# Optimization experiments

Measured on AMD Instinct MI355X. Metric: run time of the kernel, lower is better.

The kernel has to match this reference:

```python
import jax, jax.numpy as jnp
import numpy as np

EPS_LN = 1e-5

def _ln(x, g, b):
    m = x.mean(-1, keepdims=True)
    v = jnp.var(x, axis=-1, keepdims=True)
    return (x - m) * jax.lax.rsqrt(v + EPS_LN) * g + b


def _forward(x, edge_attr, lin0_w, lin0_b, enn_w1, enn_b1, enn_g1, enn_b1n,
             enn_w2, enn_b2, enn_g2, enn_b2n, conv_bias,
             gru_w_ih, gru_w_hh, gru_b_ih, gru_b_hh,
             lstm_w_ih, lstm_w_hh, lstm_b_ih, lstm_b_hh,
             lin1_w, lin1_b, lin1_g, lin1_bn, lin2_w, lin2_b,
             edge_index, target_index, target_class):
    N = x.shape[0]
    D = lin0_w.shape[0]
    src, dst = edge_index[0], edge_index[1]

    out = jax.nn.relu(x @ lin0_w.T + lin0_b)            # [N, D]
    h = out                                             # GRU hidden state

    # edge NN -> per-edge weight matrix [E, D, D] (edge_attr constant across iters)
    e1 = jax.nn.relu(_ln(edge_attr @ enn_w1.T + enn_b1, enn_g1, enn_b1n))
    ew = _ln(e1 @ enn_w2.T + enn_b2, enn_g2, enn_b2n).reshape(-1, D, D)

    counts = jnp.clip(jax.ops.segment_sum(jnp.ones_like(dst, jnp.float32), dst, num_segments=N), 1.0)[:, None]

    for _ in range(3):
        msg = jnp.einsum('ed,edo->eo', out[src], ew)     # per-edge matmul
        agg = jax.ops.segment_sum(msg, dst, num_segments=N) / counts  # scatter-mean
        m = jax.nn.relu(agg + conv_bias)
        # GRU cell (seq len 1)
        gx = m @ gru_w_ih.T + gru_b_ih
        gh = h @ gru_w_hh.T + gru_b_hh
        xr, xz, xn = jnp.split(gx, 3, axis=-1)
        hr, hz, hn = jnp.split(gh, 3, axis=-1)
        r = jax.nn.sigmoid(xr + hr)
        z = jax.nn.sigmoid(xz + hz)
        n = jnp.tanh(xn + r * hn)
        h = (1.0 - z) * n + z * h
        out = h

    # Set2Set with batch_index = arange(N) (each node is its own set), 3 steps
    idx = jnp.arange(N)
    hl = jnp.zeros((N, D), x.dtype)
    cl = jnp.zeros((N, D), x.dtype)
    q_star = jnp.zeros((N, 2 * D), x.dtype)
    for _ in range(3):
        g = q_star @ lstm_w_ih.T + lstm_b_ih + hl @ lstm_w_hh.T + lstm_b_hh
        gi, gf, gg, go = jnp.split(g, 4, axis=-1)
        cl = jax.nn.sigmoid(gf) * cl + jax.nn.sigmoid(gi) * jnp.tanh(gg)
        hl = jax.nn.sigmoid(go) * jnp.tanh(cl)
        q = hl
        e = (out * q[idx]).sum(-1, keepdims=True)
        emax = jax.ops.segment_max(e, idx, num_segments=N)
        a = jnp.exp(e - emax[idx])
        a = a / (jax.ops.segment_sum(a, idx, num_segments=N)[idx] + 1e-16)
        r_pool = jax.ops.segment_sum(a * out, idx, num_segments=N)
        q_star = jnp.concatenate([q, r_pool], axis=-1)

    a0, a1 = target_index[0], target_index[1]
    cat = jnp.concatenate([out[a0], out[a1], q_star[a0], q_star[a1]], axis=-1)  # [P, 6D]
    p = jax.nn.relu(_ln(cat @ lin1_w.T + lin1_b, lin1_g, lin1_bn))
    p = p @ lin2_w.T + lin2_b                           # [P, 8]
    return jnp.take_along_axis(p, target_class[:, None], axis=1)[:, 0]


def setup_inputs() -> dict:
    N, E, P, F, D = 10000, 20000, 15000, 16, 64
    ks = iter(jax.random.split(jax.random.key(0), 40))
    def nrm(shape, s=0.1):
        return jax.random.normal(next(ks), shape, jnp.float32) * s
    return {
        'x': jax.random.normal(next(ks), (N, F), jnp.float32),
        'edge_attr': jax.random.normal(next(ks), (E, 4), jnp.float32),
        'lin0_w': nrm((D, F)), 'lin0_b': jnp.zeros((D,), jnp.float32),
        'enn_w1': nrm((128, 4)), 'enn_b1': jnp.zeros((128,), jnp.float32),
        'enn_g1': jnp.ones((128,), jnp.float32), 'enn_b1n': jnp.zeros((128,), jnp.float32),
        'enn_w2': nrm((D * D, 128), 0.05), 'enn_b2': jnp.zeros((D * D,), jnp.float32),
        'enn_g2': jnp.ones((D * D,), jnp.float32), 'enn_b2n': jnp.zeros((D * D,), jnp.float32),
        'conv_bias': jnp.zeros((D,), jnp.float32),
        'gru_w_ih': nrm((3 * D, D)), 'gru_w_hh': nrm((3 * D, D)),
        'gru_b_ih': jnp.zeros((3 * D,), jnp.float32), 'gru_b_hh': jnp.zeros((3 * D,), jnp.float32),
        'lstm_w_ih': nrm((4 * D, 2 * D)), 'lstm_w_hh': nrm((4 * D, D)),
        'lstm_b_ih': jnp.zeros((4 * D,), jnp.float32), 'lstm_b_hh': jnp.zeros((4 * D,), jnp.float32),
        'lin1_w': nrm((D, 6 * D)), 'lin1_b': jnp.zeros((D,), jnp.float32),
        'lin1_g': jnp.ones((D,), jnp.float32), 'lin1_bn': jnp.zeros((D,), jnp.float32),
        'lin2_w': nrm((8, D)), 'lin2_b': jnp.zeros((8,), jnp.float32),
        'edge_index': jax.random.randint(next(ks), (2, E), 0, N),
        'target_index': jax.random.randint(next(ks), (2, P), 0, N),
        'target_class': jax.random.randint(next(ks), (P,), 0, 8),
    }


def reference(x, edge_attr, lin0_w, lin0_b, enn_w1, enn_b1, enn_g1, enn_b1n,
              enn_w2, enn_b2, enn_g2, enn_b2n, conv_bias,
              gru_w_ih, gru_w_hh, gru_b_ih, gru_b_hh,
              lstm_w_ih, lstm_w_hh, lstm_b_ih, lstm_b_hh,
              lin1_w, lin1_b, lin1_g, lin1_bn, lin2_w, lin2_b,
              edge_index, target_index, target_class):
    return _forward(x, edge_attr, lin0_w, lin0_b, enn_w1, enn_b1, enn_g1, enn_b1n,
                    enn_w2, enn_b2, enn_g2, enn_b2n, conv_bias,
                    gru_w_ih, gru_w_hh, gru_b_ih, gru_b_hh,
                    lstm_w_ih, lstm_w_hh, lstm_b_ih, lstm_b_hh,
                    lin1_w, lin1_b, lin1_g, lin1_bn, lin2_w, lin2_b,
                    edge_index, target_index, target_class)
```

## Files before the change

kernel.cpp:

```cpp
#include <hip/hip_runtime.h>
#include <hip/hip_bf16.h>

#define EPS_LN 1e-5f

typedef __attribute__((ext_vector_type(8))) short bf16x8;
typedef __attribute__((ext_vector_type(4))) float f32x4;

__device__ __forceinline__ float dot4(float4 a, float4 b) {
    return a.x * b.x + a.y * b.y + a.z * b.z + a.w * b.w;
}
__device__ __forceinline__ float sigmoidf_(float x) { return 1.0f / (1.0f + expf(-x)); }

__device__ __forceinline__ float bfu2f(unsigned short u) {
    unsigned v = ((unsigned)u) << 16;
    float f;
    __builtin_memcpy(&f, &v, 4);
    return f;
}
__device__ __forceinline__ unsigned short f2bfu(float f) {
    __hip_bfloat16 h = __float2bfloat16(f);
    unsigned short u;
    __builtin_memcpy(&u, &h, 2);
    return u;
}
__device__ __forceinline__ unsigned pack2bf(float a, float b) {
    return (unsigned)f2bfu(a) | ((unsigned)f2bfu(b) << 16);
}

__global__ void init_kernel(const float* __restrict__ x, const float* __restrict__ w,
                            const float* __restrict__ b, float* __restrict__ h,
                            const int* __restrict__ ei, float* __restrict__ counts,
                            int N, int E) {
    int id = blockIdx.x * blockDim.x + threadIdx.x;
    if (id < N * 64) {
        int n = id >> 6, o = id & 63;
        const float* xr = x + n * 16;
        const float* wr = w + o * 16;
        float acc = b[o];
#pragma unroll
        for (int k = 0; k < 16; k++) acc += xr[k] * wr[k];
        h[id] = fmaxf(acc, 0.0f);
    }
    if (id < E) atomicAdd(&counts[ei[E + id]], 1.0f);
}

__global__ __launch_bounds__(128) void edge_nn1_kernel(
    const float* __restrict__ ea, const float* __restrict__ w1, const float* __restrict__ b1,
    const float* __restrict__ g1, const float* __restrict__ b1n,
    unsigned short* __restrict__ e1h, unsigned short* __restrict__ e1l, int E) {
    int e = blockIdx.x, j = threadIdx.x;
    float a0 = ea[e * 4 + 0], a1 = ea[e * 4 + 1], a2 = ea[e * 4 + 2], a3 = ea[e * 4 + 3];
    const float* wr = w1 + j * 4;
    float z = b1[j] + a0 * wr[0] + a1 * wr[1] + a2 * wr[2] + a3 * wr[3];
    float s = z, s2 = z * z;
#pragma unroll
    for (int m = 32; m >= 1; m >>= 1) { s += __shfl_xor(s, m); s2 += __shfl_xor(s2, m); }
    __shared__ float ls[2], ls2[2];
    int wv = j >> 6;
    if ((j & 63) == 0) { ls[wv] = s; ls2[wv] = s2; }
    __syncthreads();
    float S = ls[0] + ls[1], S2 = ls2[0] + ls2[1];
    float mu = S * (1.0f / 128.0f);
    float var = fmaxf(S2 * (1.0f / 128.0f) - mu * mu, 0.0f);
    float inv = rsqrtf(var + EPS_LN);
    float v = fmaxf((z - mu) * inv * g1[j] + b1n[j], 0.0f);
    unsigned short hi = f2bfu(v);
    unsigned short lo = f2bfu(v - bfu2f(hi));
    e1h[e * 128 + j] = hi;
    e1l[e * 128 + j] = lo;
}

__global__ __launch_bounds__(128) void mpart_kernel(const float* __restrict__ w2,
                                                    const float* __restrict__ b2,
                                                    const float* __restrict__ g2,
                                                    unsigned short* __restrict__ w2g,
                                                    float* __restrict__ b2g,
                                                    float* __restrict__ pMT, float* __restrict__ pv,
                                                    float* __restrict__ pcw, float* __restrict__ psb,
                                                    float* __restrict__ pc) {
    __shared__ float wL[16][128];
    __shared__ float b2L[16];
    int t = threadIdx.x, b = blockIdx.x;
#pragma unroll
    for (int i = 0; i < 16; i++) {
        int idx = t + i * 128;
        wL[idx >> 7][idx & 127] = w2[(size_t)(b * 16 + (idx >> 7)) * 128 + (idx & 127)];
    }
    if (t < 16) b2L[t] = b2[b * 16 + t];
    __syncthreads();
#pragma unroll
    for (int o = 0; o < 16; o++) {
        int row = b * 16 + o;
        w2g[(size_t)row * 128 + t] = f2bfu(wL[o][t] * g2[row]);
    }
    if (t < 16) b2g[b * 16 + t] = b2L[t] * g2[b * 16 + t];
    int j = t;
    float wj[16];
#pragma unroll
    for (int o = 0; o < 16; o++) wj[o] = wL[o][j];
    float pvj = 0.f, pcwj = 0.f;
#pragma unroll
    for (int o = 0; o < 16; o++) { pvj += wj[o] * b2L[o]; pcwj += wj[o]; }
    for (int i4 = 0; i4 < 32; i4++) {
        float4 a = {0.f, 0.f, 0.f, 0.f};
#pragma unroll
        for (int o = 0; o < 16; o++) {
            float4 w4 = *(const float4*)&wL[o][i4 * 4];
            a.x += wj[o] * w4.x; a.y += wj[o] * w4.y;
            a.z += wj[o] * w4.z; a.w += wj[o] * w4.w;
        }
        *(float4*)&pMT[((size_t)b * 128 + j) * 128 + i4 * 4] = a;
    }
    pv[b * 128 + j] = pvj;
    pcw[b * 128 + j] = pcwj;
    if (t == 0) {
        float sb = 0.f, cc = 0.f;
#pragma unroll
        for (int o = 0; o < 16; o++) { sb += b2L[o]; cc += b2L[o] * b2L[o]; }
        psb[b] = sb;
        pc[b] = cc;
    }
}

__global__ __launch_bounds__(256) void mreduce_kernel(const float* __restrict__ pMT,
                                                      const float* __restrict__ pv,
                                                      const float* __restrict__ pcw,
                                                      const float* __restrict__ psb,
                                                      const float* __restrict__ pc,
                                                      unsigned short* __restrict__ mb,
                                                      float* __restrict__ varr,
                                                      float* __restrict__ cw,
                                                      float* __restrict__ sbc) {
    int fid = blockIdx.x * 256 + threadIdx.x;
    float s = 0.f;
    int j = fid >> 7, i = fid & 127;
    for (int b = 0; b < 256; b++) s += pMT[((size_t)b * 128 + j) * 128 + i];
    mb[fid] = f2bfu(s);
    if (fid < 128) {
        float sv = 0.f, sc = 0.f;
        for (int b = 0; b < 256; b++) { sv += pv[b * 128 + fid]; sc += pcw[b * 128 + fid]; }
        varr[fid] = sv;
        cw[fid] = sc;
    }
    if (fid == 0) {
        float sb = 0.f, cc = 0.f;
        for (int b = 0; b < 256; b++) { sb += psb[b]; cc += pc[b]; }
        sbc[0] = sb;
        sbc[1] = cc;
    }
}

__global__ __launch_bounds__(256) void stats_kernel(
    const unsigned short* __restrict__ e1h, const unsigned short* __restrict__ e1l,
    const unsigned short* __restrict__ mb, const float* __restrict__ cw,
    const float* __restrict__ varr, const float* __restrict__ sbc,
    float* __restrict__ stats, int E) {
    __shared__ __align__(16) unsigned char smem[65536];
    const int t = threadIdx.x;
    const int eb = blockIdx.x * 64;
#pragma unroll
    for (int r = 0; r < 4; r++) {
        int idx = t + r * 256;
        int row = idx >> 4, kseg = idx & 15;
        int er = eb + row;
        if (er >= E) er = E - 1;
        uint4 vh = *(const uint4*)&e1h[(size_t)er * 128 + kseg * 8];
        uint4 vl = *(const uint4*)&e1l[(size_t)er * 128 + kseg * 8];
        int off = row * 256 + ((kseg * 16) ^ ((row & 7) << 4));
        *(uint4*)(smem + off) = vh;
        *(uint4*)(smem + 16384 + off) = vl;
    }
#pragma unroll
    for (int r = 0; r < 8; r++) {
        int idx = t + r * 256;
        int row = idx >> 4, kseg = idx & 15;
        uint4 v = *(const uint4*)&mb[(size_t)row * 128 + kseg * 8];
        *(uint4*)(smem + 32768 + row * 256 + ((kseg * 16) ^ ((row & 7) << 4))) = v;
    }
    __syncthreads();
    const int w = t >> 6, lane = t & 63;
    const int wrow = w * 16;
    const int r16 = lane & 15, kg = lane >> 4;
    f32x4 tacc[8];
#pragma unroll
    for (int nj = 0; nj < 8; nj++) tacc[nj] = (f32x4){0.f, 0.f, 0.f, 0.f};
#pragma unroll
    for (int ks = 0; ks < 4; ks++) {
        int arow = wrow + r16;
        int koff = ks * 64 + kg * 16;
        bf16x8 ah = *(const bf16x8*)(smem + arow * 256 + (koff ^ ((arow & 7) << 4)));
        bf16x8 al = *(const bf16x8*)(smem + 16384 + arow * 256 + (koff ^ ((arow & 7) << 4)));
#pragma unroll
        for (int nj = 0; nj < 8; nj++) {
            int brow = nj * 16 + r16;
            bf16x8 bf = *(const bf16x8*)(smem + 32768 + brow * 256 + (koff ^ ((brow & 7) << 4)));
            tacc[nj] = __builtin_amdgcn_mfma_f32_16x16x32_bf16(ah, bf, tacc[nj], 0, 0, 0);
            tacc[nj] = __builtin_amdgcn_mfma_f32_16x16x32_bf16(al, bf, tacc[nj], 0, 0, 0);
        }
    }
    __syncthreads();
#pragma unroll
    for (int nj = 0; nj < 8; nj++)
#pragma unroll
        for (int r = 0; r < 4; r++) {
            int row = wrow + kg * 4 + r, col = nj * 16 + r16;
            *(float*)(smem + 32768 + row * 512 + col * 4) = tacc[nj][r];
        }
    __syncthreads();
    int el = t >> 2, q = t & 3;
    float s2p = 0.f, sp = 0.f, svp = 0.f;
    for (int kk = 0; kk < 32; kk++) {
        int k = q * 32 + kk;
        int boff = el * 256 + ((2 * k) ^ ((el & 7) << 4));
        float e1v = bfu2f(*(const unsigned short*)(smem + boff)) +
                    bfu2f(*(const unsigned short*)(smem + 16384 + boff));
        float tv = *(const float*)(smem + 32768 + el * 512 + k * 4);
        s2p += tv * e1v;
        sp += e1v * cw[k];
        svp += e1v * varr[k];
    }
    s2p += __shfl_xor(s2p, 1); s2p += __shfl_xor(s2p, 2);
    sp += __shfl_xor(sp, 1);   sp += __shfl_xor(sp, 2);
    svp += __shfl_xor(svp, 1); svp += __shfl_xor(svp, 2);
    if (q == 0) {
        int e = eb + el;
        if (e < E) {
            float S = sp + sbc[0];
            float S2 = s2p + 2.f * svp + sbc[1];
            float mu = S * (1.0f / 4096.0f);
            float var = fmaxf(S2 * (1.0f / 4096.0f) - mu * mu, 0.0f);
            float inv = rsqrtf(var + EPS_LN);
            stats[e * 2 + 0] = inv;
            stats[e * 2 + 1] = mu * inv;
        }
    }
}

__global__ __launch_bounds__(256) void zgemm_final(
    const unsigned short* __restrict__ e1h,
    const unsigned short* __restrict__ w2g, const float* __restrict__ b2g,
    const float* __restrict__ g2, const float* __restrict__ b2n,
    const float* __restrict__ stats, unsigned short* __restrict__ zT, int E) {
    __shared__ __align__(16) unsigned char smem[49152];
    __shared__ float cBg[128], cGg[128], cBn[128];
    __shared__ float sInv[64], sMiv[64];
    const int t = threadIdx.x;
    const int eb = blockIdx.y * 64;
    const int cb = blockIdx.x * 128;
    const int o0 = blockIdx.x * 2;
#pragma unroll
    for (int r = 0; r < 4; r++) {
        int idx = t + r * 256;
        int row = idx >> 4, kseg = idx & 15;
        int er = eb + row;
        if (er >= E) er = E - 1;
        uint4 vh = *(const uint4*)&e1h[(size_t)er * 128 + kseg * 8];
        *(uint4*)(smem + row * 256 + ((kseg * 16) ^ ((row & 7) << 4))) = vh;
    }
#pragma unroll
    for (int r = 0; r < 8; r++) {
        int idx = t + r * 256;
        int j = idx >> 4, kseg = idx & 15;
        int srcrow = ((j & 63) << 6) + o0 + (j >> 6);
        uint4 v = *(const uint4*)&w2g[(size_t)srcrow * 128 + kseg * 8];
        *(uint4*)(smem + 16384 + j * 256 + ((kseg * 16) ^ ((j & 7) << 4))) = v;
    }
    if (t < 128) {
        int sj = ((t & 63) << 6) + o0 + (t >> 6);
        cBg[t] = b2g[sj];
        cGg[t] = g2[sj];
        cBn[t] = b2n[sj];
    } else if (t < 192) {
        int tt = t - 128;
        int eg = eb + tt;
        if (eg >= E) eg = E - 1;
        sInv[tt] = stats[eg * 2 + 0];
        sMiv[tt] = stats[eg * 2 + 1];
    }
    __syncthreads();
    const int w = t >> 6, lane = t & 63;
    const int wrow = (w >> 1) * 32, wcol = (w & 1) * 64;
    const int r16 = lane & 15, kg = lane >> 4;

    f32x4 acc[2][4];
#pragma unroll
    for (int mi = 0; mi < 2; mi++)
#pragma unroll
        for (int nj = 0; nj < 4; nj++) acc[mi][nj] = (f32x4){0.f, 0.f, 0.f, 0.f};
#pragma unroll
    for (int ks = 0; ks < 4; ks++) {
        int koff = ks * 64 + kg * 16;
        bf16x8 af[2];
#pragma unroll
        for (int mi = 0; mi < 2; mi++) {
            int row = wrow + mi * 16 + r16;
            af[mi] = *(const bf16x8*)(smem + row * 256 + (koff ^ ((row & 7) << 4)));
        }
        bf16x8 bf[4];
#pragma unroll
        for (int nj = 0; nj < 4; nj++) {
            int row = wcol + nj * 16 + r16;
            bf[nj] = *(const bf16x8*)(smem + 16384 + row * 256 + (koff ^ ((row & 7) << 4)));
        }
#pragma unroll
        for (int mi = 0; mi < 2; mi++)
#pragma unroll
            for (int nj = 0; nj < 4; nj++)
                acc[mi][nj] = __builtin_amdgcn_mfma_f32_16x16x32_bf16(
                    bf[nj], af[mi], acc[mi][nj], 0, 0, 0);
    }
#pragma unroll
    for (int mi = 0; mi < 2; mi++) {
        int e_local = wrow + mi * 16 + r16;
        int e = eb + e_local;
        float inv = sInv[e_local], miv = sMiv[e_local];
        bool ok = (e < E);
#pragma unroll
        for (int nj = 0; nj < 4; nj++) {
            int j0 = wcol + nj * 16 + kg * 4;
            float4 bg4 = *(const float4*)&cBg[j0];
            float4 gg4 = *(const float4*)&cGg[j0];
            float4 bn4 = *(const float4*)&cBn[j0];
            ushort4 sv;
            sv.x = f2bfu(inv * (acc[mi][nj][0] + bg4.x) - miv * gg4.x + bn4.x);
            sv.y = f2bfu(inv * (acc[mi][nj][1] + bg4.y) - miv * gg4.y + bn4.y);
            sv.z = f2bfu(inv * (acc[mi][nj][2] + bg4.z) - miv * gg4.z + bn4.z);
            sv.w = f2bfu(inv * (acc[mi][nj][3] + bg4.w) - miv * gg4.w + bn4.w);
            if (ok) *(ushort4*)&zT[(size_t)e * 4096 + cb + j0] = sv;
        }
    }
}

__global__ __launch_bounds__(256) void msg_kernel(const unsigned short* __restrict__ zT,
                                                  const float* __restrict__ h,
                                                  const int* __restrict__ ei,
                                                  float* __restrict__ agg, int E) {
    int t = threadIdx.x;
    int el = t >> 6, o = t & 63;
    int e = blockIdx.x * 4 + el;
    __shared__ float sL[4][64];
    int src = ei[e];
    int dstn = ei[E + e];
    sL[el][o] = h[src * 64 + o];
    __syncthreads();
    float acc = 0.f;
    const uint4* zp = (const uint4*)(zT + (size_t)e * 4096 + o * 64);
#pragma unroll
    for (int q = 0; q < 8; q++) {
        uint4 v = zp[q];
        const float* hp = &sL[el][q * 8];
        acc += __uint_as_float(v.x << 16) * hp[0] + __uint_as_float(v.x & 0xffff0000u) * hp[1];
        acc += __uint_as_float(v.y << 16) * hp[2] + __uint_as_float(v.y & 0xffff0000u) * hp[3];
        acc += __uint_as_float(v.z << 16) * hp[4] + __uint_as_float(v.z & 0xffff0000u) * hp[5];
        acc += __uint_as_float(v.w << 16) * hp[6] + __uint_as_float(v.w & 0xffff0000u) * hp[7];
    }
    atomicAdd(&agg[(size_t)dstn * 64 + o], acc);
}

__global__ __launch_bounds__(192) void gru_kernel(
    const float* __restrict__ agg, const float* __restrict__ counts, const float* __restrict__ cbias,
    const float* __restrict__ wih, const float* __restrict__ whh,
    const float* __restrict__ bih, const float* __restrict__ bhh, float* __restrict__ h, int N) {
    int t = threadIdx.x;
    int nb = blockIdx.x * 8;
    __shared__ __align__(16) float mL[8][64], hL[8][64], gxL[8][192], ghL[8][192];
    for (int idx = t; idx < 512; idx += 192) {
        int n = idx >> 6, k = idx & 63;
        int node = nb + n;
        float cnt = fmaxf(counts[node], 1.0f);
        mL[n][k] = fmaxf(agg[node * 64 + k] / cnt + cbias[k], 0.0f);
        hL[n][k] = h[node * 64 + k];
    }
    __syncthreads();
    {
        int j = t;
        float ax[8], ah[8];
#pragma unroll
        for (int n = 0; n < 8; n++) { ax[n] = 0.f; ah[n] = 0.f; }
        const float4* wi = (const float4*)(wih + j * 64);
        const float4* wh = (const float4*)(whh + j * 64);
#pragma unroll 4
        for (int k4 = 0; k4 < 16; k4++) {
            float4 wiv = wi[k4], whv = wh[k4];
#pragma unroll
            for (int n = 0; n < 8; n++) {
                ax[n] += dot4(wiv, *(const float4*)&mL[n][k4 * 4]);
                ah[n] += dot4(whv, *(const float4*)&hL[n][k4 * 4]);
            }
        }
        float bi = bih[j], bh = bhh[j];
#pragma unroll
        for (int n = 0; n < 8; n++) { gxL[n][j] = ax[n] + bi; ghL[n][j] = ah[n] + bh; }
    }
    __syncthreads();
    for (int idx = t; idx < 512; idx += 192) {
        int n = idx >> 6, k = idx & 63;
        int node = nb + n;
        float r = sigmoidf_(gxL[n][k] + ghL[n][k]);
        float zz = sigmoidf_(gxL[n][64 + k] + ghL[n][64 + k]);
        float nn = tanhf(gxL[n][128 + k] + r * ghL[n][128 + k]);
        h[node * 64 + k] = (1.0f - zz) * nn + zz * hL[n][k];
    }
}

__global__ __launch_bounds__(256) void coutprep_kernel(
    const float* __restrict__ h, const float* __restrict__ wih, const float* __restrict__ whh,
    const float* __restrict__ bih, const float* __restrict__ bhh,
    float* __restrict__ cout, float* __restrict__ wc,
    float* __restrict__ hl, float* __restrict__ cl, int N) {
    int t = threadIdx.x, nb = blockIdx.x * 8;
    __shared__ __align__(16) float oL[8][64];
    for (int idx = t; idx < 512; idx += 256) {
        int n = idx >> 6, k = idx & 63;
        oL[n][k] = h[(nb + n) * 64 + k];
    }
    __syncthreads();
    {
        float acc[8];
#pragma unroll
        for (int n = 0; n < 8; n++) acc[n] = 0.f;
        const float* wr = wih + t * 128 + 64;
#pragma unroll 4
        for (int k4 = 0; k4 < 16; k4++) {
            float4 w4 = *(const float4*)&wr[k4 * 4];
#pragma unroll
            for (int n = 0; n < 8; n++) acc[n] += dot4(w4, *(const float4*)&oL[n][k4 * 4]);
        }
#pragma unroll
        for (int n = 0; n < 8; n++) cout[(size_t)(nb + n) * 256 + t] = acc[n];
    }
    if (blockIdx.x < 64) {
        int id = blockIdx.x * 256 + t;
        int j = id >> 6, k = id & 63;
        wc[id] = wih[j * 128 + k] + whh[id];
    }
    if (t < 64) {
        float gi = bih[t] + bhh[t];
        float gg = bih[128 + t] + bhh[128 + t];
        float go = bih[192 + t] + bhh[192 + t];
        float c0 = sigmoidf_(gi) * tanhf(gg);
        float h0 = sigmoidf_(go) * tanhf(c0);
#pragma unroll
        for (int n = 0; n < 8; n++) {
            cl[(nb + n) * 64 + t] = c0;
            hl[(nb + n) * 64 + t] = h0;
        }
    }
}

__global__ __launch_bounds__(256) void lstm_step_kernel(const float* __restrict__ wc,
                                                        const float* __restrict__ bih,
                                                        const float* __restrict__ bhh,
                                                        const float* __restrict__ cout,
                                                        float* __restrict__ hl,
                                                        float* __restrict__ cl, int N) {
    int t = threadIdx.x, nb = blockIdx.x * 8;
    __shared__ __align__(16) float hlL[8][64];
    __shared__ float gL[8][256];
    for (int idx = t; idx < 512; idx += 256) {
        int n = idx >> 6, k = idx & 63;
        hlL[n][k] = hl[(nb + n) * 64 + k];
    }
    __syncthreads();
    {
        float acc[8];
#pragma unroll
        for (int n = 0; n < 8; n++) acc[n] = 0.f;
        const float4* w4p = (const float4*)(wc + t * 64);
#pragma unroll 4
        for (int k4 = 0; k4 < 16; k4++) {
            float4 w4 = w4p[k4];
#pragma unroll
            for (int n = 0; n < 8; n++) acc[n] += dot4(w4, *(const float4*)&hlL[n][k4 * 4]);
        }
        float bs = bih[t] + bhh[t];
#pragma unroll
        for (int n = 0; n < 8; n++) gL[n][t] = acc[n] + cout[(size_t)(nb + n) * 256 + t] + bs;
    }
    __syncthreads();
    for (int idx = t; idx < 512; idx += 256) {
        int n = idx >> 6, k = idx & 63;
        int node = nb + n;
        float gi = gL[n][k], gf = gL[n][64 + k], gg = gL[n][128 + k], go = gL[n][192 + k];
        float c = sigmoidf_(gf) * cl[node * 64 + k] + sigmoidf_(gi) * tanhf(gg);
        cl[node * 64 + k] = c;
        hl[node * 64 + k] = sigmoidf_(go) * tanhf(c);
    }
}

__global__ __launch_bounds__(256) void head_kernel(
    const float* __restrict__ h, const float* __restrict__ hl, const int* __restrict__ ti,
    const int* __restrict__ tc, const float* __restrict__ w1, const float* __restrict__ b1,
    const float* __restrict__ g1, const float* __restrict__ bn1, const float* __restrict__ w2,
    const float* __restrict__ b2, float* __restrict__ out, int P) {
    __shared__ uint2 w1q[6144];
    __shared__ float catL[4][384];
    int t = threadIdx.x;
    const float4* w1f4 = (const float4*)w1;
#pragma unroll
    for (int i = 0; i < 24; i++) {
        int f = t + i * 256;
        float4 v = w1f4[f];
        int j = f / 96, k4 = f - j * 96;
        w1q[k4 * 64 + j] = make_uint2(pack2bf(v.x, v.y), pack2bf(v.z, v.w));
    }
    int j = t & 63, pl = t >> 6;
    float b1j = b1[j], g1j = g1[j], bnj = bn1[j];
    __syncthreads();

    for (int pb = blockIdx.x * 4; pb < P; pb += gridDim.x * 4) {
#pragma unroll
        for (int i = 0; i < 6; i++) {
            int idx = t + i * 256;
            int p = idx / 384, kk = idx - p * 384;
            int pair = pb + p;
            if (pair >= P) pair = P - 1;
            int a0 = ti[pair], a1 = ti[P + pair];
            int s = kk >> 6, k = kk & 63;
            float v;
            if (s == 0 || s == 3) v = h[a0 * 64 + k];
            else if (s == 1 || s == 5) v = h[a1 * 64 + k];
            else if (s == 2) v = hl[a0 * 64 + k];
            else v = hl[a1 * 64 + k];
            catL[p][kk] = v;
        }
        __syncthreads();
        int pair = pb + pl;
        float acc = b1j;
#pragma unroll 8
        for (int k4 = 0; k4 < 96; k4++) {
            uint2 wv = w1q[k4 * 64 + j];
            float4 c = *(const float4*)&catL[pl][k4 * 4];
            acc += __uint_as_float(wv.x << 16) * c.x + __uint_as_float(wv.x & 0xffff0000u) * c.y;
            acc += __uint_as_float(wv.y << 16) * c.z + __uint_as_float(wv.y & 0xffff0000u) * c.w;
        }
        float s1 = acc, s2v = acc * acc;
#pragma unroll
        for (int m = 32; m >= 1; m >>= 1) { s1 += __shfl_xor(s1, m); s2v += __shfl_xor(s2v, m); }
        float mu = s1 * (1.0f / 64.0f);
        float var = fmaxf(s2v * (1.0f / 64.0f) - mu * mu, 0.0f);
        float p1 = fmaxf((acc - mu) * rsqrtf(var + EPS_LN) * g1j + bnj, 0.0f);
        int cls = tc[pair < P ? pair : P - 1];
        float part = p1 * w2[cls * 64 + j];
#pragma unroll
        for (int m = 32; m >= 1; m >>= 1) part += __shfl_xor(part, m);
        if (j == 0 && pair < P) out[pair] = part + b2[cls];
        __syncthreads();
    }
}

extern "C" void kernel_launch(void* const* d_in, const int* in_sizes, int n_in,
                              void* d_out, int out_size, void* d_ws, size_t ws_size,
                              hipStream_t stream) {
    const float* x = (const float*)d_in[0];
    const float* edge_attr = (const float*)d_in[1];
    const float* lin0_w = (const float*)d_in[2];
    const float* lin0_b = (const float*)d_in[3];
    const float* enn_w1 = (const float*)d_in[4];
    const float* enn_b1 = (const float*)d_in[5];
    const float* enn_g1 = (const float*)d_in[6];
    const float* enn_b1n = (const float*)d_in[7];
    const float* enn_w2 = (const float*)d_in[8];
    const float* enn_b2 = (const float*)d_in[9];
    const float* enn_g2 = (const float*)d_in[10];
    const float* enn_b2n = (const float*)d_in[11];
    const float* conv_bias = (const float*)d_in[12];
    const float* gru_w_ih = (const float*)d_in[13];
    const float* gru_w_hh = (const float*)d_in[14];
    const float* gru_b_ih = (const float*)d_in[15];
    const float* gru_b_hh = (const float*)d_in[16];
    const float* lstm_w_ih = (const float*)d_in[17];
    const float* lstm_w_hh = (const float*)d_in[18];
    const float* lstm_b_ih = (const float*)d_in[19];
    const float* lstm_b_hh = (const float*)d_in[20];
    const float* lin1_w = (const float*)d_in[21];
    const float* lin1_b = (const float*)d_in[22];
    const float* lin1_g = (const float*)d_in[23];
    const float* lin1_bn = (const float*)d_in[24];
    const float* lin2_w = (const float*)d_in[25];
    const float* lin2_b = (const float*)d_in[26];
    const int* edge_index = (const int*)d_in[27];
    const int* target_index = (const int*)d_in[28];
    const int* target_class = (const int*)d_in[29];

    const int N = in_sizes[0] / 16;
    const int E = in_sizes[27] / 2;
    const int P = in_sizes[29];

    size_t off = 0;
    auto carve = [&](size_t bytes) {
        void* p = (char*)d_ws + off;
        off += (bytes + 255) & ~(size_t)255;
        return p;
    };
    unsigned short* zbuf = (unsigned short*)carve((size_t)E * 4096 * 2);
    unsigned short* e1h = (unsigned short*)carve((size_t)E * 128 * 2);
    unsigned short* e1l = (unsigned short*)carve((size_t)E * 128 * 2);
    unsigned short* w2g = (unsigned short*)carve((size_t)4096 * 128 * 2);
    float* b2g = (float*)carve((size_t)4096 * 4);
    float* hbuf = (float*)carve((size_t)N * 64 * 4);
    float* counts = (float*)carve((size_t)N * 4 + (size_t)3 * N * 64 * 4);
    float* agg0 = counts + N;
    float* agg1 = agg0 + (size_t)N * 64;
    float* agg2 = agg1 + (size_t)N * 64;
    float* hl = (float*)carve((size_t)N * 64 * 4);
    float* cl = (float*)carve((size_t)N * 64 * 4);
    float* cout_b = (float*)carve((size_t)N * 256 * 4);
    float* wc = (float*)carve((size_t)256 * 64 * 4);
    float* stats = (float*)carve((size_t)E * 2 * 4);
    unsigned short* mb = (unsigned short*)carve((size_t)128 * 128 * 2);
    float* varr = (float*)carve((size_t)128 * 4);
    float* cw = (float*)carve((size_t)128 * 4);
    float* sbc = (float*)carve((size_t)2 * 4);
    float* pv = (float*)carve((size_t)256 * 128 * 4);
    float* pcw = (float*)carve((size_t)256 * 128 * 4);
    float* psb = (float*)carve((size_t)256 * 4);
    float* pc = (float*)carve((size_t)256 * 4);
    float* pMT = (float*)carve((size_t)256 * 128 * 128 * 4);
    (void)ws_size;

    hipMemsetAsync(counts, 0, (size_t)N * 4 + (size_t)3 * N * 64 * 4, stream);
    init_kernel<<<(N * 64 + 255) / 256, 256, 0, stream>>>(x, lin0_w, lin0_b, hbuf, edge_index,
                                                          counts, N, E);
    edge_nn1_kernel<<<E, 128, 0, stream>>>(edge_attr, enn_w1, enn_b1, enn_g1, enn_b1n, e1h, e1l, E);
    mpart_kernel<<<256, 128, 0, stream>>>(enn_w2, enn_b2, enn_g2, w2g, b2g, pMT, pv, pcw, psb, pc);
    mreduce_kernel<<<64, 256, 0, stream>>>(pMT, pv, pcw, psb, pc, mb, varr, cw, sbc);
    stats_kernel<<<(E + 63) / 64, 256, 0, stream>>>(e1h, e1l, mb, cw, varr, sbc, stats, E);
    {
        dim3 g(32, (E + 63) / 64);
        zgemm_final<<<g, 256, 0, stream>>>(e1h, w2g, b2g, enn_g2, enn_b2n, stats, zbuf, E);
    }

    float* aggs[3] = {agg0, agg1, agg2};
    for (int it = 0; it < 3; it++) {
        msg_kernel<<<E / 4, 256, 0, stream>>>(zbuf, hbuf, edge_index, aggs[it], E);
        gru_kernel<<<N / 8, 192, 0, stream>>>(aggs[it], counts, conv_bias, gru_w_ih, gru_w_hh,
                                              gru_b_ih, gru_b_hh, hbuf, N);
    }

    coutprep_kernel<<<N / 8, 256, 0, stream>>>(hbuf, lstm_w_ih, lstm_w_hh, lstm_b_ih, lstm_b_hh,
                                               cout_b, wc, hl, cl, N);
    lstm_step_kernel<<<N / 8, 256, 0, stream>>>(wc, lstm_b_ih, lstm_b_hh, cout_b, hl, cl, N);
    lstm_step_kernel<<<N / 8, 256, 0, stream>>>(wc, lstm_b_ih, lstm_b_hh, cout_b, hl, cl, N);

    head_kernel<<<512, 256, 0, stream>>>(hbuf, hl, target_index, target_class, lin1_w, lin1_b,
                                         lin1_g, lin1_bn, lin2_w, lin2_b, (float*)d_out, P);
}
```

Baseline: 388.7 us.

## Fuse first message pass into edge weight GEMM epilogue and relayout zT for coalescing

The first message-passing iteration now runs inside the zgemm_final epilogue. Each block dots its freshly computed fp32 edge-weight values with the source node's hidden state and atomically adds the result into the first aggregation buffer, which removes one msg_kernel launch and one full read of the large per-edge weight tensor. The zT layout is also changed so that msg_kernel lanes read consecutive 16-byte chunks, which should coalesce the memory accesses. In exchange, the GEMM epilogue gains gathers of h rows, cross-lane shuffles and atomics, and the first iteration now uses unrounded fp32 weights while the later two use bf16.

```diff
diff --git a/kernel.cpp b/kernel.cpp
--- a/kernel.cpp
+++ b/kernel.cpp
@@ -240,13 +240,15 @@
     const unsigned short* __restrict__ e1h,
     const unsigned short* __restrict__ w2g, const float* __restrict__ b2g,
     const float* __restrict__ g2, const float* __restrict__ b2n,
-    const float* __restrict__ stats, unsigned short* __restrict__ zT, int E) {
+    const float* __restrict__ stats, const float* __restrict__ h1,
+    const int* __restrict__ ei, float* __restrict__ agg1,
+    unsigned short* __restrict__ zT, int E) {
     __shared__ __align__(16) unsigned char smem[49152];
     __shared__ float cBg[128], cGg[128], cBn[128];
     __shared__ float sInv[64], sMiv[64];
+    __shared__ int sSrc[64], sDst[64];
     const int t = threadIdx.x;
     const int eb = blockIdx.y * 64;
-    const int cb = blockIdx.x * 128;
     const int o0 = blockIdx.x * 2;
 #pragma unroll
     for (int r = 0; r < 4; r++) {
@@ -276,10 +278,17 @@
         if (eg >= E) eg = E - 1;
         sInv[tt] = stats[eg * 2 + 0];
         sMiv[tt] = stats[eg * 2 + 1];
+    } else {
+        int tt = t - 192;
+        int eg = eb + tt;
+        if (eg >= E) eg = E - 1;
+        sSrc[tt] = ei[eg];
+        sDst[tt] = ei[E + eg];
     }
     __syncthreads();
     const int w = t >> 6, lane = t & 63;
     const int wrow = (w >> 1) * 32, wcol = (w & 1) * 64;
+    const int og = o0 + (w & 1);
     const int r16 = lane & 15, kg = lane >> 4;
 
     f32x4 acc[2][4];
@@ -315,19 +324,29 @@
         int e = eb + e_local;
         float inv = sInv[e_local], miv = sMiv[e_local];
         bool ok = (e < E);
+        int src = sSrc[e_local];
+        float pm = 0.f;
 #pragma unroll
         for (int nj = 0; nj < 4; nj++) {
             int j0 = wcol + nj * 16 + kg * 4;
+            int d0 = j0 & 63;
             float4 bg4 = *(const float4*)&cBg[j0];
             float4 gg4 = *(const float4*)&cGg[j0];
             float4 bn4 = *(const float4*)&cBn[j0];
+            float v0 = inv * (acc[mi][nj][0] + bg4.x) - miv * gg4.x + bn4.x;
+            float v1 = inv * (acc[mi][nj][1] + bg4.y) - miv * gg4.y + bn4.y;
+            float v2 = inv * (acc[mi][nj][2] + bg4.z) - miv * gg4.z + bn4.z;
+            float v3 = inv * (acc[mi][nj][3] + bg4.w) - miv * gg4.w + bn4.w;
+            float4 h4 = *(const float4*)&h1[(size_t)src * 64 + d0];
+            pm += v0 * h4.x + v1 * h4.y + v2 * h4.z + v3 * h4.w;
             ushort4 sv;
-            sv.x = f2bfu(inv * (acc[mi][nj][0] + bg4.x) - miv * gg4.x + bn4.x);
-            sv.y = f2bfu(inv * (acc[mi][nj][1] + bg4.y) - miv * gg4.y + bn4.y);
-            sv.z = f2bfu(inv * (acc[mi][nj][2] + bg4.z) - miv * gg4.z + bn4.z);
-            sv.w = f2bfu(inv * (acc[mi][nj][3] + bg4.w) - miv * gg4.w + bn4.w);
-            if (ok) *(ushort4*)&zT[(size_t)e * 4096 + cb + j0] = sv;
-        }
+            sv.x = f2bfu(v0); sv.y = f2bfu(v1); sv.z = f2bfu(v2); sv.w = f2bfu(v3);
+            if (ok)
+                *(ushort4*)&zT[(size_t)e * 4096 + ((d0 >> 3) << 9) + og * 8 + (d0 & 7)] = sv;
+        }
+        pm += __shfl_xor(pm, 16);
+        pm += __shfl_xor(pm, 32);
+        if (ok && kg == 0) atomicAdd(&agg1[(size_t)sDst[e_local] * 64 + og], pm);
     }
 }
 
@@ -336,25 +355,25 @@
                                                   const int* __restrict__ ei,
                                                   float* __restrict__ agg, int E) {
     int t = threadIdx.x;
-    int el = t >> 6, o = t & 63;
-    int e = blockIdx.x * 4 + el;
-    __shared__ float sL[4][64];
+    int w = t >> 6, lane = t & 63;
+    int e = blockIdx.x * 4 + w;
+    __shared__ float hL[4][64];
     int src = ei[e];
     int dstn = ei[E + e];
-    sL[el][o] = h[src * 64 + o];
+    hL[w][lane] = h[(size_t)src * 64 + lane];
     __syncthreads();
     float acc = 0.f;
-    const uint4* zp = (const uint4*)(zT + (size_t)e * 4096 + o * 64);
+    const uint4* zp = (const uint4*)(zT + (size_t)e * 4096);
 #pragma unroll
     for (int q = 0; q < 8; q++) {
-        uint4 v = zp[q];
-        const float* hp = &sL[el][q * 8];
+        uint4 v = zp[q * 64 + lane];
+        const float* hp = &hL[w][q * 8];
         acc += __uint_as_float(v.x << 16) * hp[0] + __uint_as_float(v.x & 0xffff0000u) * hp[1];
         acc += __uint_as_float(v.y << 16) * hp[2] + __uint_as_float(v.y & 0xffff0000u) * hp[3];
         acc += __uint_as_float(v.z << 16) * hp[4] + __uint_as_float(v.z & 0xffff0000u) * hp[5];
         acc += __uint_as_float(v.w << 16) * hp[6] + __uint_as_float(v.w & 0xffff0000u) * hp[7];
     }
-    atomicAdd(&agg[(size_t)dstn * 64 + o], acc);
+    atomicAdd(&agg[(size_t)dstn * 64 + lane], acc);
 }
 
 __global__ __launch_bounds__(192) void gru_kernel(
@@ -628,11 +647,14 @@
     stats_kernel<<<(E + 63) / 64, 256, 0, stream>>>(e1h, e1l, mb, cw, varr, sbc, stats, E);
     {
         dim3 g(32, (E + 63) / 64);
-        zgemm_final<<<g, 256, 0, stream>>>(e1h, w2g, b2g, enn_g2, enn_b2n, stats, zbuf, E);
-    }
-
-    float* aggs[3] = {agg0, agg1, agg2};
-    for (int it = 0; it < 3; it++) {
+        zgemm_final<<<g, 256, 0, stream>>>(e1h, w2g, b2g, enn_g2, enn_b2n, stats, hbuf,
+                                           edge_index, agg0, zbuf, E);
+    }
+
+    gru_kernel<<<N / 8, 192, 0, stream>>>(agg0, counts, conv_bias, gru_w_ih, gru_w_hh,
+                                          gru_b_ih, gru_b_hh, hbuf, N);
+    float* aggs[2] = {agg1, agg2};
+    for (int it = 0; it < 2; it++) {
         msg_kernel<<<E / 4, 256, 0, stream>>>(zbuf, hbuf, edge_index, aggs[it], E);
         gru_kernel<<<N / 8, 192, 0, stream>>>(aggs[it], counts, conv_bias, gru_w_ih, gru_w_hh,
                                               gru_b_ih, gru_b_hh, hbuf, N);
```

Result: slower. 428.4 us (+10.2%).
